# Optimization experiments

Measured on AMD Instinct MI355X. Metric: run time of the kernel, lower is better.

## Reference

```python
import jax, jax.numpy as jnp
import numpy as np

E = 1024
H = 16
HD = 64
LN_EPS = 1e-5


def _layernorm(x, g, b):
    mu = jnp.mean(x, axis=-1, keepdims=True)
    var = jnp.mean((x - mu) ** 2, axis=-1, keepdims=True)
    return (x - mu) * jax.lax.rsqrt(var + LN_EPS) * g + b


def _positional(L):
    # PositionalEncoding: stepper = 1/10000^(arange(0,E,2)/E); cat(sin, cos) -> [L, E]
    stepper = 1.0 / (10000.0 ** (jnp.arange(0, E, 2, dtype=jnp.float32) / E))
    args = jnp.arange(L, dtype=jnp.float32)[:, None] * stepper[None, :]  # [L, E/2]
    return jnp.concatenate([jnp.sin(args), jnp.cos(args)], axis=1)  # [L, E]


def setup_inputs() -> dict:
    key = jax.random.key(0)
    ks = jax.random.split(key, 8)
    s = 1.0 / np.sqrt(E)
    return {
        "sequences": jax.random.normal(ks[0], (4, 2048, E), dtype=jnp.float32),
        "W_q": jax.random.normal(ks[1], (E, E), dtype=jnp.float32) * s,
        "W_k": jax.random.normal(ks[2], (E, E), dtype=jnp.float32) * s,
        "W_v": jax.random.normal(ks[3], (E, E), dtype=jnp.float32) * s,
        "W_o": jax.random.normal(ks[4], (E, E), dtype=jnp.float32) * s,
        "ln1_g": jnp.ones((E,), jnp.float32),
        "ln1_b": jnp.zeros((E,), jnp.float32),
        "lin_W": jax.random.normal(ks[5], (E, E), dtype=jnp.float32) * s,  # torch Linear weight [out,in]
        "lin_b": jnp.zeros((E,), jnp.float32),
        "ln2_g": jnp.ones((E,), jnp.float32),
        "ln2_b": jnp.zeros((E,), jnp.float32),
    }


def reference(sequences, W_q, W_k, W_v, W_o, ln1_g, ln1_b, lin_W, lin_b, ln2_g, ln2_b):
    B, L, _ = sequences.shape
    x = sequences + _positional(L)[None]  # add positional embeddings
    # projections (no bias)
    q = (x @ W_q).reshape(B, L, H, HD).transpose(0, 2, 1, 3)  # [B,H,L,hd]
    k = (x @ W_k).reshape(B, L, H, HD).transpose(0, 2, 1, 3)
    v = (x @ W_v).reshape(B, L, H, HD).transpose(0, 2, 1, 3)
    # linear (softmax-free) attention: (Q K^T / sqrt(hd)) V
    scores = jnp.einsum("bhqd,bhkd->bhqk", q, k) / jnp.sqrt(jnp.float32(HD))
    ctx = jnp.einsum("bhqk,bhkd->bhqd", scores, v)
    ctx = ctx.transpose(0, 2, 1, 3).reshape(B, L, E)
    attn_out = ctx @ W_o
    h = _layernorm(x + attn_out, ln1_g, ln1_b)
    ff = jax.nn.relu(h @ lin_W.T + lin_b)
    return _layernorm(ff + h, ln2_g, ln2_b)
```

## Files before the change

kernel.cpp:

```cpp
#include <hip/hip_runtime.h>
#include <cstdint>

typedef unsigned short u16;
typedef __bf16 bf16x8 __attribute__((ext_vector_type(8)));
typedef float f32x4 __attribute__((ext_vector_type(4)));

__device__ __forceinline__ u16 f2bf(float f) {
    unsigned u = __float_as_uint(f);
    u += 0x7fffu + ((u >> 16) & 1u);
    return (u16)(u >> 16);
}
__device__ __forceinline__ float bf2f(u16 h) {
    return __uint_as_float(((unsigned)h) << 16);
}

__device__ __forceinline__ void lds16(const void* g, void* l) {
    __builtin_amdgcn_global_load_lds(
        (const __attribute__((address_space(1))) void*)g,
        (__attribute__((address_space(3))) void*)l, 16, 0, 0);
}

__device__ __forceinline__ float pos_term(int l, int e) {
    const float c = -13.287712379549449f / 512.0f;
    int ii = e & 511;
    float st  = exp2f(c * (float)ii);
    float arg = (float)l * st;
    return (e < 512) ? sinf(arg) : cosf(arg);
}

__global__ __launch_bounds__(256) void prep_x(const float* __restrict__ seq,
                                              u16* __restrict__ xb) {
    size_t i = (size_t)blockIdx.x * 256 + threadIdx.x;
    int e4 = (int)(i & 255) * 4;
    int l  = (int)((i >> 8) & 2047);
    float4 s = ((const float4*)seq)[i];
    float v[4] = {s.x, s.y, s.z, s.w};
#pragma unroll
    for (int j = 0; j < 4; j++) v[j] += pos_term(l, e4 + j);
    ushort4 ob; ob.x = f2bf(v[0]); ob.y = f2bf(v[1]); ob.z = f2bf(v[2]); ob.w = f2bf(v[3]);
    ((ushort4*)xb)[i] = ob;
}

__global__ void prep_w(const float* __restrict__ wq, const float* __restrict__ wk,
                       const float* __restrict__ wv, const float* __restrict__ wl,
                       u16* __restrict__ wt) {
    int mat = blockIdx.z;
    const float* src = (mat == 0) ? wq : (mat == 1) ? wk : (mat == 2) ? wv : wl;
    u16* dst = wt + (size_t)mat * 1024 * 1024;
    int tx = threadIdx.x, ty = threadIdx.y;
    if (mat == 0 || mat == 3) {
        int col = blockIdx.x * 32 + tx, row0 = blockIdx.y * 32;
#pragma unroll
        for (int j = 0; j < 32; j += 8)
            dst[(size_t)(row0 + ty + j) * 1024 + col] = f2bf(src[(size_t)(row0 + ty + j) * 1024 + col]);
    } else {
        __shared__ float tile[32][33];
        int col = blockIdx.x * 32 + tx, row0 = blockIdx.y * 32;
#pragma unroll
        for (int j = 0; j < 32; j += 8)
            tile[ty + j][tx] = src[(size_t)(row0 + ty + j) * 1024 + col];
        __syncthreads();
        int col2 = blockIdx.y * 32 + tx, row20 = blockIdx.x * 32;
#pragma unroll
        for (int j = 0; j < 32; j += 8)
            dst[(size_t)(row20 + ty + j) * 1024 + col2] = f2bf(tile[tx][ty + j]);
    }
}

__global__ __launch_bounds__(512) void gemm256(const u16* __restrict__ A,
                                               const u16* __restrict__ Bt,
                                               u16* __restrict__ C,
                                               int N, int K, int lda) {
    __shared__ __align__(16) u16 lds[65536];
    const int t = threadIdx.x;
    const int ntn = N >> 8;
    const int nwg = gridDim.x;
    int bid = (int)blockIdx.x;
    bid = (bid & 7) * (nwg >> 3) + (bid >> 3);
    const int tm = bid / ntn, tn = bid - tm * ntn;
    const size_t m0 = (size_t)tm << 8, n0 = (size_t)tn << 8;
    const int w = t >> 6, lane = t & 63;
    const int wr = w >> 2, wc = w & 3;

    const int r0 = t >> 3;
    const int ksrc = (t & 7) ^ (r0 & 7);
    const u16* sA0 = A + (m0 + r0) * (size_t)lda + ksrc * 8;
    const u16* sA1 = sA0 + (size_t)128 * lda;
    const u16* sB0 = Bt + (n0 + r0) * (size_t)K + ksrc * 8;
    const u16* sB1 = sB0 + (size_t)128 * K;
    const size_t stA = (size_t)64 * lda, stB = (size_t)64 * K;

#define STAGE(bb, hh, src, str, ko)                                           \
    do {                                                                      \
        u16* d_ = lds + (bb) * 32768 + (hh) * 8192 + (w << 9);                \
        lds16((src) + (ko), d_);                                              \
        lds16((src) + (ko) + (str), d_ + 4096);                               \
    } while (0)

    const int kx = lane & 7;
    const int ks0 = (((lane >> 4) ^ kx) << 3);
    const int ks1 = (((4 + (lane >> 4)) ^ kx) << 3);
    const int arow = (wr << 7) + (lane & 15);
    const int brow = (wc << 6) + (lane & 15);

    f32x4 acc[8][4];
#pragma unroll
    for (int i = 0; i < 8; i++)
#pragma unroll
        for (int j = 0; j < 4; j++)
#pragma unroll
            for (int r = 0; r < 4; r++) acc[i][j][r] = 0.0f;

    const int NT = K >> 6;
    STAGE(0, 0, sA0, stA, 0); STAGE(0, 1, sA1, stA, 0);
    STAGE(0, 2, sB0, stB, 0); STAGE(0, 3, sB1, stB, 0);
    if (NT > 1) {
        STAGE(1, 0, sA0, stA, 64); STAGE(1, 1, sA1, stA, 64);
        asm volatile("s_waitcnt vmcnt(4)" ::: "memory");
    } else {
        asm volatile("s_waitcnt vmcnt(0)" ::: "memory");
    }
    __builtin_amdgcn_s_barrier();
    asm volatile("" ::: "memory");

    for (int kt = 0; kt < NT; kt++) {
        const int b = kt & 1;
        const u16* Lb = lds + b * 32768;
        const size_t ko1 = (size_t)(kt + 1) << 6;
        const size_t ko2 = (size_t)(kt + 2) << 6;
        const bool p1 = (kt + 1 < NT), p2 = (kt + 2 < NT);
        bf16x8 af[4][2], b0[2][2], b1[2][2];

#pragma unroll
        for (int i = 0; i < 4; i++) {
            const int ar = (arow + i * 16) << 6;
            af[i][0] = *reinterpret_cast<const bf16x8*>(Lb + ar + ks0);
            af[i][1] = *reinterpret_cast<const bf16x8*>(Lb + ar + ks1);
        }
#pragma unroll
        for (int j = 0; j < 2; j++) {
            const int br = 16384 + ((brow + j * 16) << 6);
            b0[j][0] = *reinterpret_cast<const bf16x8*>(Lb + br + ks0);
            b0[j][1] = *reinterpret_cast<const bf16x8*>(Lb + br + ks1);
        }
        if (p1) STAGE(b ^ 1, 2, sB0, stB, ko1);
        asm volatile("s_waitcnt lgkmcnt(8)" ::: "memory");
        __builtin_amdgcn_s_barrier();
        asm volatile("s_waitcnt lgkmcnt(0)" ::: "memory");
        __builtin_amdgcn_sched_barrier(0);
        __builtin_amdgcn_s_setprio(1);
#pragma unroll
        for (int kc = 0; kc < 2; kc++)
#pragma unroll
            for (int i = 0; i < 4; i++)
#pragma unroll
                for (int j = 0; j < 2; j++)
                    acc[i][j] = __builtin_amdgcn_mfma_f32_16x16x32_bf16(
                        af[i][kc], b0[j][kc], acc[i][j], 0, 0, 0);
        __builtin_amdgcn_s_setprio(0);
        asm volatile("" ::: "memory");
        __builtin_amdgcn_s_barrier();

#pragma unroll
        for (int j = 0; j < 2; j++) {
            const int br = 16384 + ((brow + 32 + j * 16) << 6);
            b1[j][0] = *reinterpret_cast<const bf16x8*>(Lb + br + ks0);
            b1[j][1] = *reinterpret_cast<const bf16x8*>(Lb + br + ks1);
        }
        if (p1) STAGE(b ^ 1, 3, sB1, stB, ko1);
        __builtin_amdgcn_s_barrier();
        asm volatile("s_waitcnt lgkmcnt(0)" ::: "memory");
        __builtin_amdgcn_sched_barrier(0);
        __builtin_amdgcn_s_setprio(1);
#pragma unroll
        for (int kc = 0; kc < 2; kc++)
#pragma unroll
            for (int i = 0; i < 4; i++)
#pragma unroll
                for (int j = 0; j < 2; j++)
                    acc[i][2 + j] = __builtin_amdgcn_mfma_f32_16x16x32_bf16(
                        af[i][kc], b1[j][kc], acc[i][2 + j], 0, 0, 0);
        __builtin_amdgcn_s_setprio(0);
        asm volatile("" ::: "memory");
        __builtin_amdgcn_s_barrier();

#pragma unroll
        for (int i = 0; i < 4; i++) {
            const int ar = (arow + 64 + i * 16) << 6;
            af[i][0] = *reinterpret_cast<const bf16x8*>(Lb + ar + ks0);
            af[i][1] = *reinterpret_cast<const bf16x8*>(Lb + ar + ks1);
        }
        __builtin_amdgcn_s_barrier();
        asm volatile("s_waitcnt lgkmcnt(0)" ::: "memory");
        __builtin_amdgcn_sched_barrier(0);
        __builtin_amdgcn_s_setprio(1);
#pragma unroll
        for (int kc = 0; kc < 2; kc++)
#pragma unroll
            for (int i = 0; i < 4; i++)
#pragma unroll
                for (int j = 0; j < 2; j++)
                    acc[4 + i][j] = __builtin_amdgcn_mfma_f32_16x16x32_bf16(
                        af[i][kc], b0[j][kc], acc[4 + i][j], 0, 0, 0);
        __builtin_amdgcn_s_setprio(0);
        asm volatile("" ::: "memory");
        __builtin_amdgcn_s_barrier();

        if (p2) {
            STAGE(b, 0, sA0, stA, ko2);
            STAGE(b, 1, sA1, stA, ko2);
            asm volatile("s_waitcnt vmcnt(4)" ::: "memory");
        } else if (p1) {
            asm volatile("s_waitcnt vmcnt(0)" ::: "memory");
        }
        __builtin_amdgcn_s_barrier();
        __builtin_amdgcn_s_setprio(1);
#pragma unroll
        for (int kc = 0; kc < 2; kc++)
#pragma unroll
            for (int i = 0; i < 4; i++)
#pragma unroll
                for (int j = 0; j < 2; j++)
                    acc[4 + i][2 + j] = __builtin_amdgcn_mfma_f32_16x16x32_bf16(
                        af[i][kc], b1[j][kc], acc[4 + i][2 + j], 0, 0, 0);
        __builtin_amdgcn_s_setprio(0);
        asm volatile("" ::: "memory");
        __builtin_amdgcn_s_barrier();
    }
#undef STAGE

    const int crow = (lane >> 4) << 2, ccol = lane & 15;
#pragma unroll
    for (int i = 0; i < 8; i++)
#pragma unroll
        for (int j = 0; j < 4; j++) {
            size_t row = m0 + (wr << 7) + (i << 4) + crow;
            size_t col = n0 + (wc << 6) + (j << 4) + ccol;
#pragma unroll
            for (int r = 0; r < 4; r++)
                C[(row + r) * (size_t)N + col] = f2bf(acc[i][j][r]);
        }
}

template <int EPI>
__global__ __launch_bounds__(512) void gemm8p(const u16* __restrict__ A,
                                              const u16* __restrict__ Bt,
                                              void* __restrict__ Cv,
                                              const float* __restrict__ bias,
                                              int N, int K, int lda, size_t bstride) {
    __shared__ __align__(16) u16 lds[49152];
    const int t = threadIdx.x;
    const int ntn = N >> 8;
    const int nwg = gridDim.x;
    int bid = (int)blockIdx.x;
    bid = (bid & 7) * (nwg >> 3) + (bid >> 3);
    const int tm = bid / ntn, tn = bid - tm * ntn;
    const size_t m0 = (size_t)tm << 7, n0 = (size_t)tn << 8;
    const int w = t >> 6, lane = t & 63;
    const int wr = w >> 2, wc = w & 3;
    const u16* Bt_e = Bt + (bstride ? (m0 >> 11) * bstride : 0);

    const int r0 = t >> 3;
    const int ksrc = (t & 7) ^ (r0 & 7);
    const u16* sA0 = A + (m0 + r0) * (size_t)lda + ksrc * 8;
    const u16* sA1 = sA0 + (size_t)64 * lda;
    const u16* sB0 = Bt_e + (n0 + r0) * (size_t)K + ksrc * 8;
    const u16* sB1 = sB0 + (size_t)64 * K;
    const u16* sB2 = sB0 + (size_t)128 * K;
    const u16* sB3 = sB0 + (size_t)192 * K;
    u16* dstW = lds + (w << 9);

    const int ao = ((wr << 6) | (lane & 15)) << 6;
    const int bo = 8192 + ((((wc << 6) | (lane & 15))) << 6);
    const int kx = lane & 7;
    const int ks0 = (((lane >> 4) ^ kx) << 3);
    const int ks1 = (((4 + (lane >> 4)) ^ kx) << 3);

    f32x4 acc[4][4];
#pragma unroll
    for (int i = 0; i < 4; i++)
#pragma unroll
        for (int j = 0; j < 4; j++)
#pragma unroll
            for (int r = 0; r < 4; r++) acc[i][j][r] = 0.0f;

    const int NT = K >> 6;
    lds16(sA0, dstW);          lds16(sA1, dstW + 4096);
    lds16(sB0, dstW + 8192);   lds16(sB1, dstW + 12288);
    lds16(sB2, dstW + 16384);  lds16(sB3, dstW + 20480);

    for (int kt = 0; kt < NT; kt++) {
        const int b = kt & 1;
        asm volatile("" ::: "memory");
        if (kt + 1 < NT) {
            const size_t ko = (size_t)(kt + 1) << 6;
            u16* d = dstW + (b ^ 1) * 24576;
            lds16(sA0 + ko, d);          lds16(sA1 + ko, d + 4096);
            lds16(sB0 + ko, d + 8192);   lds16(sB1 + ko, d + 12288);
            lds16(sB2 + ko, d + 16384);  lds16(sB3 + ko, d + 20480);
            asm volatile("s_waitcnt vmcnt(6)" ::: "memory");
        } else {
            asm volatile("s_waitcnt vmcnt(0)" ::: "memory");
        }
        __builtin_amdgcn_s_barrier();
        asm volatile("" ::: "memory");
        const u16* Lb = lds + b * 24576;
#pragma unroll
        for (int kc = 0; kc < 2; kc++) {
            const int ksl = kc ? ks1 : ks0;
            bf16x8 af[4], bfr[4];
#pragma unroll
            for (int i = 0; i < 4; i++)
                af[i] = *reinterpret_cast<const bf16x8*>(Lb + ao + i * 1024 + ksl);
#pragma unroll
            for (int j = 0; j < 4; j++)
                bfr[j] = *reinterpret_cast<const bf16x8*>(Lb + bo + j * 1024 + ksl);
            __builtin_amdgcn_s_setprio(1);
#pragma unroll
            for (int i = 0; i < 4; i++)
#pragma unroll
                for (int j = 0; j < 4; j++)
                    acc[i][j] = __builtin_amdgcn_mfma_f32_16x16x32_bf16(af[i], bfr[j], acc[i][j], 0, 0, 0);
            __builtin_amdgcn_s_setprio(0);
        }
        asm volatile("" ::: "memory");
        __builtin_amdgcn_s_barrier();
    }

    const int crow = (lane >> 4) << 2, ccol = lane & 15;
#pragma unroll
    for (int i = 0; i < 4; i++)
#pragma unroll
        for (int j = 0; j < 4; j++) {
            size_t row = m0 + (wr << 6) + (i << 4) + crow;
            size_t col = n0 + (wc << 6) + (j << 4) + ccol;
#pragma unroll
            for (int r = 0; r < 4; r++) {
                float v = acc[i][j][r];
                if (EPI == 3) { v += bias[col]; v = fmaxf(v, 0.0f); }
                ((u16*)Cv)[(row + r) * (size_t)N + col] = f2bf(v);
            }
        }
}

__global__ __launch_bounds__(256) void ktv_kernel(const u16* __restrict__ kv,
                                                  float* __restrict__ part) {
    const int bh = blockIdx.x, split = blockIdx.y;
    const int b = bh >> 4, h = bh & 15;
    const u16* Kp = kv + (size_t)b * 2048 * 2048 + h * 64;
    const u16* Vp = Kp + 1024;
    __shared__ float ks[8][64], vs[8][64];
    float acc[16];
#pragma unroll
    for (int i = 0; i < 16; i++) acc[i] = 0.0f;
    const int t = threadIdx.x, r = t >> 4, c = t & 15;
    const int lr = t >> 5, lc = (t & 31) * 2;
    for (int l0 = split * 128; l0 < split * 128 + 128; l0 += 8) {
        unsigned kk = *(const unsigned*)(Kp + (size_t)(l0 + lr) * 2048 + lc);
        unsigned vv = *(const unsigned*)(Vp + (size_t)(l0 + lr) * 2048 + lc);
        ks[lr][lc] = bf2f((u16)kk); ks[lr][lc + 1] = bf2f((u16)(kk >> 16));
        vs[lr][lc] = bf2f((u16)vv); vs[lr][lc + 1] = bf2f((u16)(vv >> 16));
        __syncthreads();
#pragma unroll
        for (int i = 0; i < 8; i++) {
            float kvr[4], vw[4];
#pragma unroll
            for (int a = 0; a < 4; a++) { kvr[a] = ks[i][r + 16 * a]; vw[a] = vs[i][c + 16 * a]; }
#pragma unroll
            for (int a = 0; a < 4; a++)
#pragma unroll
                for (int q = 0; q < 4; q++) acc[a * 4 + q] += kvr[a] * vw[q];
        }
        __syncthreads();
    }
    float* o = part + ((size_t)split * 64 + bh) * 4096;
#pragma unroll
    for (int a = 0; a < 4; a++)
#pragma unroll
        for (int q = 0; q < 4; q++) o[(r + 16 * a) * 64 + (c + 16 * q)] = acc[a * 4 + q];
}

__global__ __launch_bounds__(256) void ktv_reduce(const float* __restrict__ part,
                                                  float* __restrict__ ktv) {
    int i = blockIdx.x * 256 + threadIdx.x;
    float s = 0.0f;
#pragma unroll
    for (int sp = 0; sp < 16; sp++) s += part[(size_t)sp * 262144 + i];
    ktv[i] = s;
}

__global__ __launch_bounds__(256) void wprime_kernel(const float* __restrict__ ktv,
                                                     const float* __restrict__ Wo,
                                                     u16* __restrict__ wp) {
    const int n = blockIdx.x * 256 + threadIdx.x;
    const int h = blockIdx.y, b = blockIdx.z;
    const float* kt = ktv + ((size_t)(b * 16 + h) << 12);
    float acc[64];
#pragma unroll
    for (int i = 0; i < 64; i++) acc[i] = 0.0f;
    for (int j = 0; j < 64; j++) {
        float w = Wo[(size_t)(h * 64 + j) * 1024 + n];
#pragma unroll
        for (int i = 0; i < 64; i++) acc[i] += kt[i * 64 + j] * w;
    }
    u16* o = wp + ((size_t)b << 20) + (size_t)n * 1024 + h * 64;
    u16 ob[64];
#pragma unroll
    for (int i = 0; i < 64; i++) ob[i] = f2bf(acc[i] * 0.125f);
#pragma unroll
    for (int i = 0; i < 8; i++)
        ((uint4*)o)[i] = ((const uint4*)ob)[i];
}

__global__ __launch_bounds__(256) void ln1_kernel(const u16* __restrict__ xb,
                                                  const u16* __restrict__ attn,
                                                  const float* __restrict__ g,
                                                  const float* __restrict__ be,
                                                  u16* __restrict__ outB) {
    __shared__ float sm[4];
    const int row = blockIdx.x, t = threadIdx.x;
    const ushort4 xv = ((const ushort4*)(xb + (size_t)row * 1024))[t];
    const ushort4 av = ((const ushort4*)(attn + (size_t)row * 1024))[t];
    float x0 = bf2f(xv.x) + bf2f(av.x), x1 = bf2f(xv.y) + bf2f(av.y);
    float x2 = bf2f(xv.z) + bf2f(av.z), x3 = bf2f(xv.w) + bf2f(av.w);
    float s = x0 + x1 + x2 + x3;
#pragma unroll
    for (int off = 32; off > 0; off >>= 1) s += __shfl_down(s, off);
    if ((t & 63) == 0) sm[t >> 6] = s;
    __syncthreads();
    const float mean = (sm[0] + sm[1] + sm[2] + sm[3]) * (1.0f / 1024.0f);
    __syncthreads();
    x0 -= mean; x1 -= mean; x2 -= mean; x3 -= mean;
    float s2 = x0 * x0 + x1 * x1 + x2 * x2 + x3 * x3;
#pragma unroll
    for (int off = 32; off > 0; off >>= 1) s2 += __shfl_down(s2, off);
    if ((t & 63) == 0) sm[t >> 6] = s2;
    __syncthreads();
    const float var = (sm[0] + sm[1] + sm[2] + sm[3]) * (1.0f / 1024.0f);
    const float rs = rsqrtf(var + 1e-5f);
    const float4 gv = ((const float4*)g)[t];
    const float4 bv = ((const float4*)be)[t];
    ushort4 ob;
    ob.x = f2bf(x0 * rs * gv.x + bv.x);
    ob.y = f2bf(x1 * rs * gv.y + bv.y);
    ob.z = f2bf(x2 * rs * gv.z + bv.z);
    ob.w = f2bf(x3 * rs * gv.w + bv.w);
    ((ushort4*)(outB + (size_t)row * 1024))[t] = ob;
}

__global__ __launch_bounds__(256) void ln2_kernel(const u16* __restrict__ ff,
                                                  const u16* __restrict__ h1,
                                                  const float* __restrict__ g,
                                                  const float* __restrict__ be,
                                                  float* __restrict__ outF) {
    __shared__ float sm[4];
    const int row = blockIdx.x, t = threadIdx.x;
    const ushort4 fv = ((const ushort4*)(ff + (size_t)row * 1024))[t];
    const ushort4 hv = ((const ushort4*)(h1 + (size_t)row * 1024))[t];
    float x0 = bf2f(fv.x) + bf2f(hv.x), x1 = bf2f(fv.y) + bf2f(hv.y);
    float x2 = bf2f(fv.z) + bf2f(hv.z), x3 = bf2f(fv.w) + bf2f(hv.w);
    float s = x0 + x1 + x2 + x3;
#pragma unroll
    for (int off = 32; off > 0; off >>= 1) s += __shfl_down(s, off);
    if ((t & 63) == 0) sm[t >> 6] = s;
    __syncthreads();
    const float mean = (sm[0] + sm[1] + sm[2] + sm[3]) * (1.0f / 1024.0f);
    __syncthreads();
    x0 -= mean; x1 -= mean; x2 -= mean; x3 -= mean;
    float s2 = x0 * x0 + x1 * x1 + x2 * x2 + x3 * x3;
#pragma unroll
    for (int off = 32; off > 0; off >>= 1) s2 += __shfl_down(s2, off);
    if ((t & 63) == 0) sm[t >> 6] = s2;
    __syncthreads();
    const float var = (sm[0] + sm[1] + sm[2] + sm[3]) * (1.0f / 1024.0f);
    const float rs = rsqrtf(var + 1e-5f);
    const float4 gv = ((const float4*)g)[t];
    const float4 bv = ((const float4*)be)[t];
    float4 o;
    o.x = x0 * rs * gv.x + bv.x;
    o.y = x1 * rs * gv.y + bv.y;
    o.z = x2 * rs * gv.z + bv.z;
    o.w = x3 * rs * gv.w + bv.w;
    ((float4*)(outF + (size_t)row * 1024))[t] = o;
}

extern "C" void kernel_launch(void* const* d_in, const int* in_sizes, int n_in,
                              void* d_out, int out_size, void* d_ws, size_t ws_size,
                              hipStream_t stream) {
    const float* seq = (const float*)d_in[0];
    const float* Wq  = (const float*)d_in[1];
    const float* Wk  = (const float*)d_in[2];
    const float* Wv  = (const float*)d_in[3];
    const float* Wo  = (const float*)d_in[4];
    const float* g1  = (const float*)d_in[5];
    const float* b1  = (const float*)d_in[6];
    const float* Wl  = (const float*)d_in[7];
    const float* bl  = (const float*)d_in[8];
    const float* g2  = (const float*)d_in[9];
    const float* b2  = (const float*)d_in[10];

    char* ws = (char*)d_ws;
    const size_t MB = 1024 * 1024;
    u16*   x_bf  = (u16*)(ws + 0);
    u16*   wt    = (u16*)(ws + 16 * MB);
    u16*   kv    = (u16*)(ws + 24 * MB);
    float* kpart = (float*)(ws + 56 * MB);
    u16*   attn  = (u16*)(ws + 56 * MB);
    float* ktv   = (float*)(ws + 72 * MB);
    u16*   wpr   = (u16*)(ws + 73 * MB);
    u16*   wcomb = (u16*)(ws + 81 * MB);
    u16*   h1b   = (u16*)(ws + 89 * MB);
    u16*   ffb   = (u16*)(ws + 105 * MB);

    prep_x<<<dim3(8192), dim3(256), 0, stream>>>(seq, x_bf);
    prep_w<<<dim3(32, 32, 4), dim3(32, 8), 0, stream>>>(Wq, Wk, Wv, Wl, wt);
    gemm256<<<dim3(256), dim3(512), 0, stream>>>(x_bf, wt + (size_t)1 * MB, kv,
                                                 2048, 1024, 1024);
    ktv_kernel<<<dim3(64, 16), dim3(256), 0, stream>>>(kv, kpart);
    ktv_reduce<<<dim3(1024), dim3(256), 0, stream>>>(kpart, ktv);
    wprime_kernel<<<dim3(4, 16, 4), dim3(256), 0, stream>>>(ktv, Wo, wpr);
    gemm8p<2><<<dim3(128), dim3(512), 0, stream>>>(wpr, wt, wcomb, nullptr,
                                                   1024, 1024, 1024, 0);
    gemm8p<2><<<dim3(256), dim3(512), 0, stream>>>(x_bf, wcomb, attn, nullptr,
                                                   1024, 1024, 1024, (size_t)1024 * 1024);
    ln1_kernel<<<dim3(8192), dim3(256), 0, stream>>>(x_bf, attn, g1, b1, h1b);
    gemm8p<3><<<dim3(256), dim3(512), 0, stream>>>(h1b, wt + (size_t)3 * MB, ffb,
                                                   bl, 1024, 1024, 1024, 0);
    ln2_kernel<<<dim3(8192), dim3(256), 0, stream>>>(ffb, h1b, g2, b2, (float*)d_out);
}
```

Before: 201.5 us.

## Fuse prep kernels, ktv reduce into wprime, fold residual identity into combined weight

Merges the x and weight preparation kernels into a single launch, and folds the split-K reduction of K^T V into the W' kernel by summing partials in shared memory. A new 128-tile GEMM builds the combined weight with an identity added to its diagonal, so the attention GEMM outputs x + attn directly and LN1 reads one tensor instead of two. The gemm256 pipeline is also rewritten to stage the full next tile at the top of each iteration with fewer barriers. The goal is fewer launches, less memory traffic and less sync overhead. In exchange, the ktv partial sums are recomputed redundantly per block, and the residual now comes out of a bf16 GEMM, which may change rounding.

```diff
diff --git a/kernel.cpp b/kernel.cpp
--- a/kernel.cpp
+++ b/kernel.cpp
@@ -28,39 +28,45 @@
     return (e < 512) ? sinf(arg) : cosf(arg);
 }
 
-__global__ __launch_bounds__(256) void prep_x(const float* __restrict__ seq,
-                                              u16* __restrict__ xb) {
-    size_t i = (size_t)blockIdx.x * 256 + threadIdx.x;
-    int e4 = (int)(i & 255) * 4;
-    int l  = (int)((i >> 8) & 2047);
-    float4 s = ((const float4*)seq)[i];
-    float v[4] = {s.x, s.y, s.z, s.w};
-#pragma unroll
-    for (int j = 0; j < 4; j++) v[j] += pos_term(l, e4 + j);
-    ushort4 ob; ob.x = f2bf(v[0]); ob.y = f2bf(v[1]); ob.z = f2bf(v[2]); ob.w = f2bf(v[3]);
-    ((ushort4*)xb)[i] = ob;
-}
-
-__global__ void prep_w(const float* __restrict__ wq, const float* __restrict__ wk,
-                       const float* __restrict__ wv, const float* __restrict__ wl,
-                       u16* __restrict__ wt) {
-    int mat = blockIdx.z;
+__global__ __launch_bounds__(256) void prep_all(const float* __restrict__ seq,
+                                                const float* __restrict__ wq,
+                                                const float* __restrict__ wk,
+                                                const float* __restrict__ wv,
+                                                const float* __restrict__ wl,
+                                                u16* __restrict__ xb,
+                                                u16* __restrict__ wt) {
+    const int bx = blockIdx.x;
+    if (bx < 8192) {
+        size_t i = (size_t)bx * 256 + threadIdx.x;
+        int e4 = (int)(i & 255) * 4;
+        int l  = (int)((i >> 8) & 2047);
+        float4 s = ((const float4*)seq)[i];
+        float v[4] = {s.x, s.y, s.z, s.w};
+#pragma unroll
+        for (int j = 0; j < 4; j++) v[j] += pos_term(l, e4 + j);
+        ushort4 ob; ob.x = f2bf(v[0]); ob.y = f2bf(v[1]); ob.z = f2bf(v[2]); ob.w = f2bf(v[3]);
+        ((ushort4*)xb)[i] = ob;
+        return;
+    }
+    const int idx = bx - 8192;
+    const int mat = idx >> 10, bxw = idx & 1023;
+    const int gx = bxw & 31, gy = bxw >> 5;
+    const int tx = threadIdx.x & 31, ty = threadIdx.x >> 5;
     const float* src = (mat == 0) ? wq : (mat == 1) ? wk : (mat == 2) ? wv : wl;
     u16* dst = wt + (size_t)mat * 1024 * 1024;
-    int tx = threadIdx.x, ty = threadIdx.y;
     if (mat == 0 || mat == 3) {
-        int col = blockIdx.x * 32 + tx, row0 = blockIdx.y * 32;
+        int col = gx * 32 + tx, row0 = gy * 32;
 #pragma unroll
         for (int j = 0; j < 32; j += 8)
             dst[(size_t)(row0 + ty + j) * 1024 + col] = f2bf(src[(size_t)(row0 + ty + j) * 1024 + col]);
     } else {
         __shared__ float tile[32][33];
-        int col = blockIdx.x * 32 + tx, row0 = blockIdx.y * 32;
+        int col = gx * 32 + tx, row0 = gy * 32;
 #pragma unroll
         for (int j = 0; j < 32; j += 8)
             tile[ty + j][tx] = src[(size_t)(row0 + ty + j) * 1024 + col];
         __syncthreads();
-        int col2 = blockIdx.y * 32 + tx, row20 = blockIdx.x * 32;
+        int col2 = gy * 32 + tx, row20 = gx * 32;
 #pragma unroll
         for (int j = 0; j < 32; j += 8)
             dst[(size_t)(row20 + ty + j) * 1024 + col2] = f2bf(tile[tx][ty + j]);
@@ -114,115 +120,72 @@
     const int NT = K >> 6;
     STAGE(0, 0, sA0, stA, 0); STAGE(0, 1, sA1, stA, 0);
     STAGE(0, 2, sB0, stB, 0); STAGE(0, 3, sB1, stB, 0);
-    if (NT > 1) {
-        STAGE(1, 0, sA0, stA, 64); STAGE(1, 1, sA1, stA, 64);
-        asm volatile("s_waitcnt vmcnt(4)" ::: "memory");
-    } else {
-        asm volatile("s_waitcnt vmcnt(0)" ::: "memory");
-    }
-    __builtin_amdgcn_s_barrier();
-    asm volatile("" ::: "memory");
 
     for (int kt = 0; kt < NT; kt++) {
         const int b = kt & 1;
         const u16* Lb = lds + b * 32768;
-        const size_t ko1 = (size_t)(kt + 1) << 6;
-        const size_t ko2 = (size_t)(kt + 2) << 6;
-        const bool p1 = (kt + 1 < NT), p2 = (kt + 2 < NT);
+        asm volatile("" ::: "memory");
+        if (kt + 1 < NT) {
+            const size_t ko = (size_t)(kt + 1) << 6;
+            STAGE(b ^ 1, 0, sA0, stA, ko); STAGE(b ^ 1, 1, sA1, stA, ko);
+            STAGE(b ^ 1, 2, sB0, stB, ko); STAGE(b ^ 1, 3, sB1, stB, ko);
+            asm volatile("s_waitcnt vmcnt(8)" ::: "memory");
+        } else {
+            asm volatile("s_waitcnt vmcnt(0)" ::: "memory");
+        }
+        __builtin_amdgcn_s_barrier();
+        asm volatile("" ::: "memory");
+
         bf16x8 af[4][2], b0[2][2], b1[2][2];
-
+#pragma unroll
+        for (int j = 0; j < 2; j++) {
+            const int br = 16384 + ((brow + j * 16) << 6);
+            b0[j][0] = *reinterpret_cast<const bf16x8*>(Lb + br + ks0);
+            b0[j][1] = *reinterpret_cast<const bf16x8*>(Lb + br + ks1);
+        }
+#pragma unroll
+        for (int j = 0; j < 2; j++) {
+            const int br = 16384 + ((brow + 32 + j * 16) << 6);
+            b1[j][0] = *reinterpret_cast<const bf16x8*>(Lb + br + ks0);
+            b1[j][1] = *reinterpret_cast<const bf16x8*>(Lb + br + ks1);
+        }
 #pragma unroll
         for (int i = 0; i < 4; i++) {
             const int ar = (arow + i * 16) << 6;
             af[i][0] = *reinterpret_cast<const bf16x8*>(Lb + ar + ks0);
             af[i][1] = *reinterpret_cast<const bf16x8*>(Lb + ar + ks1);
         }
-#pragma unroll
-        for (int j = 0; j < 2; j++) {
-            const int br = 16384 + ((brow + j * 16) << 6);
-            b0[j][0] = *reinterpret_cast<const bf16x8*>(Lb + br + ks0);
-            b0[j][1] = *reinterpret_cast<const bf16x8*>(Lb + br + ks1);
-        }
-        if (p1) STAGE(b ^ 1, 2, sB0, stB, ko1);
-        asm volatile("s_waitcnt lgkmcnt(8)" ::: "memory");
-        __builtin_amdgcn_s_barrier();
-        asm volatile("s_waitcnt lgkmcnt(0)" ::: "memory");
-        __builtin_amdgcn_sched_barrier(0);
         __builtin_amdgcn_s_setprio(1);
 #pragma unroll
         for (int kc = 0; kc < 2; kc++)
 #pragma unroll
             for (int i = 0; i < 4; i++)
 #pragma unroll
-                for (int j = 0; j < 2; j++)
+                for (int j = 0; j < 2; j++) {
                     acc[i][j] = __builtin_amdgcn_mfma_f32_16x16x32_bf16(
                         af[i][kc], b0[j][kc], acc[i][j], 0, 0, 0);
-        __builtin_amdgcn_s_setprio(0);
-        asm volatile("" ::: "memory");
-        __builtin_amdgcn_s_barrier();
-
-#pragma unroll
-        for (int j = 0; j < 2; j++) {
-            const int br = 16384 + ((brow + 32 + j * 16) << 6);
-            b1[j][0] = *reinterpret_cast<const bf16x8*>(Lb + br + ks0);
-            b1[j][1] = *reinterpret_cast<const bf16x8*>(Lb + br + ks1);
-        }
-        if (p1) STAGE(b ^ 1, 3, sB1, stB, ko1);
-        __builtin_amdgcn_s_barrier();
-        asm volatile("s_waitcnt lgkmcnt(0)" ::: "memory");
-        __builtin_amdgcn_sched_barrier(0);
-        __builtin_amdgcn_s_setprio(1);
-#pragma unroll
-        for (int kc = 0; kc < 2; kc++)
-#pragma unroll
-            for (int i = 0; i < 4; i++)
-#pragma unroll
-                for (int j = 0; j < 2; j++)
                     acc[i][2 + j] = __builtin_amdgcn_mfma_f32_16x16x32_bf16(
                         af[i][kc], b1[j][kc], acc[i][2 + j], 0, 0, 0);
+                }
         __builtin_amdgcn_s_setprio(0);
-        asm volatile("" ::: "memory");
-        __builtin_amdgcn_s_barrier();
-
 #pragma unroll
         for (int i = 0; i < 4; i++) {
             const int ar = (arow + 64 + i * 16) << 6;
             af[i][0] = *reinterpret_cast<const bf16x8*>(Lb + ar + ks0);
             af[i][1] = *reinterpret_cast<const bf16x8*>(Lb + ar + ks1);
         }
-        __builtin_amdgcn_s_barrier();
-        asm volatile("s_waitcnt lgkmcnt(0)" ::: "memory");
-        __builtin_amdgcn_sched_barrier(0);
         __builtin_amdgcn_s_setprio(1);
 #pragma unroll
         for (int kc = 0; kc < 2; kc++)
 #pragma unroll
             for (int i = 0; i < 4; i++)
 #pragma unroll
-                for (int j = 0; j < 2; j++)
+                for (int j = 0; j < 2; j++) {
                     acc[4 + i][j] = __builtin_amdgcn_mfma_f32_16x16x32_bf16(
                         af[i][kc], b0[j][kc], acc[4 + i][j], 0, 0, 0);
-        __builtin_amdgcn_s_setprio(0);
-        asm volatile("" ::: "memory");
-        __builtin_amdgcn_s_barrier();
-
-        if (p2) {
-            STAGE(b, 0, sA0, stA, ko2);
-            STAGE(b, 1, sA1, stA, ko2);
-            asm volatile("s_waitcnt vmcnt(4)" ::: "memory");
-        } else if (p1) {
-            asm volatile("s_waitcnt vmcnt(0)" ::: "memory");
-        }
-        __builtin_amdgcn_s_barrier();
-        __builtin_amdgcn_s_setprio(1);
-#pragma unroll
-        for (int kc = 0; kc < 2; kc++)
-#pragma unroll
-            for (int i = 0; i < 4; i++)
-#pragma unroll
-                for (int j = 0; j < 2; j++)
                     acc[4 + i][2 + j] = __builtin_amdgcn_mfma_f32_16x16x32_bf16(
                         af[i][kc], b1[j][kc], acc[4 + i][2 + j], 0, 0, 0);
+                }
         __builtin_amdgcn_s_setprio(0);
         asm volatile("" ::: "memory");
         __builtin_amdgcn_s_barrier();
@@ -343,6 +306,106 @@
         }
 }
 
+template <bool ADDI>
+__global__ __launch_bounds__(256) void gemm128(const u16* __restrict__ A,
+                                               const u16* __restrict__ Bt,
+                                               u16* __restrict__ C,
+                                               int N, int K, int lda) {
+    __shared__ __align__(16) u16 lds[32768];
+    const int t = threadIdx.x;
+    const int ntn = N >> 7;
+    const int nwg = gridDim.x;
+    int bid = (int)blockIdx.x;
+    bid = (bid & 7) * (nwg >> 3) + (bid >> 3);
+    const int tm = bid / ntn, tn = bid - tm * ntn;
+    const size_t m0 = (size_t)tm << 7, n0 = (size_t)tn << 7;
+    const int w = t >> 6, lane = t & 63;
+    const int wr = w >> 1, wc = w & 1;
+
+    const int r0 = t >> 3;
+    const int ksrc = (t & 7) ^ (r0 & 7);
+    const u16* sA = A + (m0 + r0) * (size_t)lda + ksrc * 8;
+    const u16* sB = Bt + (n0 + r0) * (size_t)K + ksrc * 8;
+    const size_t stA = (size_t)32 * lda, stB = (size_t)32 * K;
+
+    const int kx = lane & 7;
+    const int ks0 = (((lane >> 4) ^ kx) << 3);
+    const int ks1 = (((4 + (lane >> 4)) ^ kx) << 3);
+    const int ao = ((wr << 6) | (lane & 15)) << 6;
+    const int bo = 8192 + ((((wc << 6) | (lane & 15))) << 6);
+
+    f32x4 acc[4][4];
+#pragma unroll
+    for (int i = 0; i < 4; i++)
+#pragma unroll
+        for (int j = 0; j < 4; j++)
+#pragma unroll
+            for (int r = 0; r < 4; r++) acc[i][j][r] = 0.0f;
+
+#define STAGE128(bb, ko)                                                      \
+    do {                                                                      \
+        u16* dA_ = lds + (bb) * 16384 + (w << 9);                             \
+        u16* dB_ = dA_ + 8192;                                                \
+        _Pragma("unroll")                                                     \
+        for (int j_ = 0; j_ < 4; j_++) {                                      \
+            lds16(sA + (ko) + j_ * stA, dA_ + j_ * 2048);                     \
+            lds16(sB + (ko) + j_ * stB, dB_ + j_ * 2048);                     \
+        }                                                                     \
+    } while (0)
+
+    const int NT = K >> 6;
+    STAGE128(0, 0);
+    for (int kt = 0; kt < NT; kt++) {
+        const int b = kt & 1;
+        asm volatile("" ::: "memory");
+        if (kt + 1 < NT) {
+            STAGE128(b ^ 1, (size_t)(kt + 1) << 6);
+            asm volatile("s_waitcnt vmcnt(8)" ::: "memory");
+        } else {
+            asm volatile("s_waitcnt vmcnt(0)" ::: "memory");
+        }
+        __builtin_amdgcn_s_barrier();
+        asm volatile("" ::: "memory");
+        const u16* Lb = lds + b * 16384;
+#pragma unroll
+        for (int kc = 0; kc < 2; kc++) {
+            const int ksl = kc ? ks1 : ks0;
+            bf16x8 af[4], bfr[4];
+#pragma unroll
+            for (int i = 0; i < 4; i++)
+                af[i] = *reinterpret_cast<const bf16x8*>(Lb + ao + i * 1024 + ksl);
+#pragma unroll
+            for (int j = 0; j < 4; j++)
+                bfr[j] = *reinterpret_cast<const bf16x8*>(Lb + bo + j * 1024 + ksl);
+            __builtin_amdgcn_s_setprio(1);
+#pragma unroll
+            for (int i = 0; i < 4; i++)
+#pragma unroll
+                for (int j = 0; j < 4; j++)
+                    acc[i][j] = __builtin_amdgcn_mfma_f32_16x16x32_bf16(af[i], bfr[j], acc[i][j], 0, 0, 0);
+            __builtin_amdgcn_s_setprio(0);
+        }
+        asm volatile("" ::: "memory");
+        __builtin_amdgcn_s_barrier();
+    }
+#undef STAGE128
+
+    const int crow = (lane >> 4) << 2, ccol = lane & 15;
+#pragma unroll
+    for (int i = 0; i < 4; i++)
+#pragma unroll
+        for (int j = 0; j < 4; j++) {
+            size_t row = m0 + (wr << 6) + (i << 4) + crow;
+            size_t col = n0 + (wc << 6) + (j << 4) + ccol;
+#pragma unroll
+            for (int r = 0; r < 4; r++) {
+                float v = acc[i][j][r];
+                if (ADDI && col == ((row + r) & 1023)) v += 1.0f;
+                C[(row + r) * (size_t)N + col] = f2bf(v);
+            }
+        }
+}
+
 __global__ __launch_bounds__(256) void ktv_kernel(const u16* __restrict__ kv,
                                                   float* __restrict__ part) {
     const int bh = blockIdx.x, split = blockIdx.y;
@@ -380,28 +443,28 @@
         for (int q = 0; q < 4; q++) o[(r + 16 * a) * 64 + (c + 16 * q)] = acc[a * 4 + q];
 }
 
-__global__ __launch_bounds__(256) void ktv_reduce(const float* __restrict__ part,
-                                                  float* __restrict__ ktv) {
-    int i = blockIdx.x * 256 + threadIdx.x;
-    float s = 0.0f;
-#pragma unroll
-    for (int sp = 0; sp < 16; sp++) s += part[(size_t)sp * 262144 + i];
-    ktv[i] = s;
-}
-
-__global__ __launch_bounds__(256) void wprime_kernel(const float* __restrict__ ktv,
-                                                     const float* __restrict__ Wo,
-                                                     u16* __restrict__ wp) {
+__global__ __launch_bounds__(256) void ktv_wp(const float* __restrict__ part,
+                                              const float* __restrict__ Wo,
+                                              u16* __restrict__ wp) {
+    __shared__ float kt[4096];
     const int n = blockIdx.x * 256 + threadIdx.x;
     const int h = blockIdx.y, b = blockIdx.z;
-    const float* kt = ktv + ((size_t)(b * 16 + h) << 12);
+    const int bh = b * 16 + h;
+    for (int e = threadIdx.x; e < 4096; e += 256) {
+        float s = 0.0f;
+#pragma unroll
+        for (int sp = 0; sp < 16; sp++)
+            s += part[(size_t)sp * 262144 + (size_t)bh * 4096 + e];
+        kt[e] = s;
+    }
+    __syncthreads();
     float acc[64];
 #pragma unroll
     for (int i = 0; i < 64; i++) acc[i] = 0.0f;
     for (int j = 0; j < 64; j++) {
-        float w = Wo[(size_t)(h * 64 + j) * 1024 + n];
-#pragma unroll
-        for (int i = 0; i < 64; i++) acc[i] += kt[i * 64 + j] * w;
+        float wv = Wo[(size_t)(h * 64 + j) * 1024 + n];
+#pragma unroll
+        for (int i = 0; i < 64; i++) acc[i] += kt[i * 64 + j] * wv;
     }
     u16* o = wp + ((size_t)b << 20) + (size_t)n * 1024 + h * 64;
     u16 ob[64];
@@ -412,17 +475,14 @@
         ((uint4*)o)[i] = ((const uint4*)ob)[i];
 }
 
-__global__ __launch_bounds__(256) void ln1_kernel(const u16* __restrict__ xb,
-                                                  const u16* __restrict__ attn,
+__global__ __launch_bounds__(256) void ln1_kernel(const u16* __restrict__ xr,
                                                   const float* __restrict__ g,
                                                   const float* __restrict__ be,
                                                   u16* __restrict__ outB) {
     __shared__ float sm[4];
     const int row = blockIdx.x, t = threadIdx.x;
-    const ushort4 xv = ((const ushort4*)(xb + (size_t)row * 1024))[t];
-    const ushort4 av = ((const ushort4*)(attn + (size_t)row * 1024))[t];
-    float x0 = bf2f(xv.x) + bf2f(av.x), x1 = bf2f(xv.y) + bf2f(av.y);
-    float x2 = bf2f(xv.z) + bf2f(av.z), x3 = bf2f(xv.w) + bf2f(av.w);
+    const ushort4 xv = ((const ushort4*)(xr + (size_t)row * 1024))[t];
+    float x0 = bf2f(xv.x), x1 = bf2f(xv.y), x2 = bf2f(xv.z), x3 = bf2f(xv.w);
     float s = x0 + x1 + x2 + x3;
 #pragma unroll
     for (int off = 32; off > 0; off >>= 1) s += __shfl_down(s, off);
@@ -501,29 +561,25 @@
 
     char* ws = (char*)d_ws;
     const size_t MB = 1024 * 1024;
-    u16*   x_bf  = (u16*)(ws + 0);
-    u16*   wt    = (u16*)(ws + 16 * MB);
-    u16*   kv    = (u16*)(ws + 24 * MB);
-    float* kpart = (float*)(ws + 56 * MB);
-    u16*   attn  = (u16*)(ws + 56 * MB);
-    float* ktv   = (float*)(ws + 72 * MB);
-    u16*   wpr   = (u16*)(ws + 73 * MB);
-    u16*   wcomb = (u16*)(ws + 81 * MB);
-    u16*   h1b   = (u16*)(ws + 89 * MB);
-    u16*   ffb   = (u16*)(ws + 105 * MB);
-
-    prep_x<<<dim3(8192), dim3(256), 0, stream>>>(seq, x_bf);
-    prep_w<<<dim3(32, 32, 4), dim3(32, 8), 0, stream>>>(Wq, Wk, Wv, Wl, wt);
+    u16*   x_bf    = (u16*)(ws + 0);
+    u16*   wt      = (u16*)(ws + 16 * MB);
+    u16*   kv      = (u16*)(ws + 24 * MB);
+    float* kpart   = (float*)(ws + 56 * MB);
+    u16*   attnres = (u16*)(ws + 56 * MB);
+    u16*   wpr     = (u16*)(ws + 72 * MB);
+    u16*   wcomb   = (u16*)(ws + 80 * MB);
+    u16*   h1b     = (u16*)(ws + 88 * MB);
+    u16*   ffb     = (u16*)(ws + 104 * MB);
+
+    prep_all<<<dim3(8192 + 4096), dim3(256), 0, stream>>>(seq, Wq, Wk, Wv, Wl, x_bf, wt);
     gemm256<<<dim3(256), dim3(512), 0, stream>>>(x_bf, wt + (size_t)1 * MB, kv,
                                                  2048, 1024, 1024);
     ktv_kernel<<<dim3(64, 16), dim3(256), 0, stream>>>(kv, kpart);
-    ktv_reduce<<<dim3(1024), dim3(256), 0, stream>>>(kpart, ktv);
-    wprime_kernel<<<dim3(4, 16, 4), dim3(256), 0, stream>>>(ktv, Wo, wpr);
-    gemm8p<2><<<dim3(128), dim3(512), 0, stream>>>(wpr, wt, wcomb, nullptr,
-                                                   1024, 1024, 1024, 0);
-    gemm8p<2><<<dim3(256), dim3(512), 0, stream>>>(x_bf, wcomb, attn, nullptr,
+    ktv_wp<<<dim3(4, 16, 4), dim3(256), 0, stream>>>(kpart, Wo, wpr);
+    gemm128<true><<<dim3(256), dim3(256), 0, stream>>>(wpr, wt, wcomb, 1024, 1024, 1024);
+    gemm8p<2><<<dim3(256), dim3(512), 0, stream>>>(x_bf, wcomb, attnres, nullptr,
                                                    1024, 1024, 1024, (size_t)1024 * 1024);
-    ln1_kernel<<<dim3(8192), dim3(256), 0, stream>>>(x_bf, attn, g1, b1, h1b);
+    ln1_kernel<<<dim3(8192), dim3(256), 0, stream>>>(attnres, g1, b1, h1b);
     gemm8p<3><<<dim3(256), dim3(512), 0, stream>>>(h1b, wt + (size_t)3 * MB, ffb,
                                                    bl, 1024, 1024, 1024, 0);
     ln2_kernel<<<dim3(8192), dim3(256), 0, stream>>>(ffb, h1b, g2, b2, (float*)d_out);
```

Measured after the change: 214.9 us. 1.07x slower.
